# Kernel optimization log

Hardware: AMD Instinct MI355X
Metric: run time of the kernel (lower is better)

The kernel has to match this reference:

```python
import jax, jax.numpy as jnp
import numpy as np

B, T, D = 4, 2048, 2048
NUM_HEADS = 16
NUM_KV_HEADS = 4
HEAD_DIM = D // NUM_HEADS  # 128
KV_GROUPS = NUM_HEADS // NUM_KV_HEADS  # 4
ROPE_THETA = 10000.0


def _rope_tables(seq_len, head_dim, theta):
    inv_freq = 1.0 / theta ** (jnp.arange(0, head_dim, 2, dtype=jnp.float32) / head_dim)
    t = jnp.arange(seq_len, dtype=jnp.float32)
    freqs = jnp.outer(t, inv_freq)  # (T, head_dim//2)
    return jnp.cos(freqs), jnp.sin(freqs)


def _apply_rotary(x, cos, sin):
    # x: (B, H, T, d); cos/sin: (T, d//2)
    d = x.shape[-1]
    x1, x2 = x[..., : d // 2], x[..., d // 2:]
    c = cos[None, None, :, :]
    s = sin[None, None, :, :]
    return jnp.concatenate([x1 * c - x2 * s, x1 * s + x2 * c], axis=-1)


def setup_inputs() -> dict:
    key = jax.random.key(0)
    kx, kq, kk, kv, ko = jax.random.split(key, 5)
    scale = 1.0 / np.sqrt(D)
    return {
        "x": jax.random.normal(kx, (B, T, D), dtype=jnp.float32),
        "Wq": jax.random.normal(kq, (NUM_HEADS * HEAD_DIM, D), dtype=jnp.float32) * scale,
        "Wk": jax.random.normal(kk, (NUM_KV_HEADS * HEAD_DIM, D), dtype=jnp.float32) * scale,
        "Wv": jax.random.normal(kv, (NUM_KV_HEADS * HEAD_DIM, D), dtype=jnp.float32) * scale,
        "Wo": jax.random.normal(ko, (D, D), dtype=jnp.float32) * scale,
    }


def reference(x, Wq, Wk, Wv, Wo):
    Bc, Tc, Dc = x.shape
    # projections (Linear with weight (out,in): y = x @ W.T)
    q = (x @ Wq.T).reshape(Bc, Tc, NUM_HEADS, HEAD_DIM).transpose(0, 2, 1, 3)
    k = (x @ Wk.T).reshape(Bc, Tc, NUM_KV_HEADS, HEAD_DIM).transpose(0, 2, 1, 3)
    v = (x @ Wv.T).reshape(Bc, Tc, NUM_KV_HEADS, HEAD_DIM).transpose(0, 2, 1, 3)

    cos, sin = _rope_tables(Tc, HEAD_DIM, ROPE_THETA)
    q = _apply_rotary(q, cos, sin)
    k = _apply_rotary(k, cos, sin)

    # grouped-query attention: broadcast KV heads instead of repeat_interleave
    # q: (B, kvH, G, T, d); k,v: (B, kvH, T, d)
    qg = q.reshape(Bc, NUM_KV_HEADS, KV_GROUPS, Tc, HEAD_DIM)
    scores = jnp.einsum("bkgtd,bksd->bkgts", qg, k) / jnp.sqrt(jnp.float32(HEAD_DIM))
    causal = jnp.tril(jnp.ones((Tc, Tc), dtype=bool))
    scores = jnp.where(causal[None, None, None], scores, jnp.float32(-jnp.inf))
    attn = jax.nn.softmax(scores, axis=-1)
    out = jnp.einsum("bkgts,bksd->bkgtd", attn, v)  # (B, kvH, G, T, d)
    out = out.reshape(Bc, NUM_HEADS, Tc, HEAD_DIM).transpose(0, 2, 1, 3).reshape(Bc, Tc, Dc)
    return out @ Wo.T
```

## Files before the change

kernel.cpp:

```cpp
#include <hip/hip_runtime.h>
#include <stdint.h>

#define B_ 4
#define T_ 2048
#define D_ 2048
#define NH_ 16
#define NKV_ 4
#define HD_ 128
#define QKVN 3072
#define SCALE_ 0.08838834764831845f

typedef unsigned short u16;
typedef __attribute__((ext_vector_type(8))) short short8;
typedef __attribute__((ext_vector_type(4))) float floatx4;

typedef __attribute__((address_space(1))) void* gas_p;
typedef __attribute__((address_space(3))) void* las_p;

__device__ __forceinline__ u16 f2bf(float f) {
  union { float f; uint32_t u; } a; a.f = f;
  uint32_t r = a.u + 0x7fffu + ((a.u >> 16) & 1u);
  return (u16)(r >> 16);
}
__device__ __forceinline__ float bf2f(u16 u) {
  union { uint32_t u; float f; } a; a.u = ((uint32_t)u) << 16;
  return a.f;
}
__device__ __forceinline__ void gl_lds16(const u16* g, u16* l) {
  __builtin_amdgcn_global_load_lds((gas_p)g, (las_p)l, 16, 0, 0);
}

__global__ void cvt_kernel(const float* __restrict__ in, u16* __restrict__ out, int n) {
  int i = blockIdx.x * 256 + threadIdx.x;
  if (i * 4 >= n) return;
  float4 v = ((const float4*)in)[i];
  union { u16 u[4]; uint2 v2; } o;
  o.u[0] = f2bf(v.x); o.u[1] = f2bf(v.y); o.u[2] = f2bf(v.z); o.u[3] = f2bf(v.w);
  ((uint2*)out)[i] = o.v2;
}

__global__ void rope_tables_kernel(float* __restrict__ tabs) {
  int i = blockIdx.x * 256 + threadIdx.x;
  if (i >= T_ * 64) return;
  int t = i >> 6, d = i & 63;
  float inv = powf(10000.0f, -(float)d / 64.0f);
  float f = (float)t * inv;
  tabs[i] = cosf(f);
  tabs[T_ * 64 + i] = sinf(f);
}

__global__ void rope_q_kernel(const u16* __restrict__ qkv, const float* __restrict__ tabs,
                              u16* __restrict__ q_r) {
  int i = blockIdx.x * 256 + threadIdx.x;
  if (i >= B_ * T_ * NH_ * 64) return;
  int d = i & 63;
  int h = (i >> 6) & 15;
  int t = (i >> 10) & 2047;
  int b = i >> 21;
  size_t row = (size_t)(b * T_ + t) * QKVN + h * HD_;
  float x1 = bf2f(qkv[row + d]);
  float x2 = bf2f(qkv[row + d + 64]);
  float c = tabs[t * 64 + d];
  float s = tabs[T_ * 64 + t * 64 + d];
  size_t ob = ((size_t)(b * NH_ + h) * T_ + t) * HD_;
  q_r[ob + d] = f2bf((x1 * c - x2 * s) * SCALE_);
  q_r[ob + d + 64] = f2bf((x1 * s + x2 * c) * SCALE_);
}

__global__ void rope_k_kernel(const u16* __restrict__ qkv, const float* __restrict__ tabs,
                              u16* __restrict__ k_r) {
  int i = blockIdx.x * 256 + threadIdx.x;
  if (i >= B_ * T_ * NKV_ * 64) return;
  int d = i & 63;
  int kh = (i >> 6) & 3;
  int t = (i >> 8) & 2047;
  int b = i >> 19;
  size_t row = (size_t)(b * T_ + t) * QKVN + D_ + kh * HD_;
  float x1 = bf2f(qkv[row + d]);
  float x2 = bf2f(qkv[row + d + 64]);
  float c = tabs[t * 64 + d];
  float s = tabs[T_ * 64 + t * 64 + d];
  size_t ob = ((size_t)(b * NKV_ + kh) * T_ + t) * HD_;
  k_r[ob + d] = f2bf(x1 * c - x2 * s);
  k_r[ob + d + 64] = f2bf(x1 * s + x2 * c);
}

__global__ void v_trans_kernel(const u16* __restrict__ qkv, u16* __restrict__ v_t) {
  __shared__ u16 tile[64 * 128];
  int bk = blockIdx.y;
  int b = bk >> 2, kh = bk & 3;
  int t0 = blockIdx.x * 64;
#pragma unroll
  for (int rep = 0; rep < 32; rep++) {
    int idx = rep * 256 + threadIdx.x;
    int tt = idx >> 7, d = idx & 127;
    tile[idx] = qkv[(size_t)(b * T_ + t0 + tt) * QKVN + D_ + 512 + kh * HD_ + d];
  }
  __syncthreads();
#pragma unroll
  for (int rep = 0; rep < 32; rep++) {
    int idx = rep * 256 + threadIdx.x;
    int d = idx >> 6, tt = idx & 63;
    v_t[((size_t)bk * HD_ + d) * T_ + t0 + tt] = tile[tt * 128 + d];
  }
}

template <int OUTF32>
__global__ __launch_bounds__(256)
void gemm_bt(const u16* __restrict__ A, const u16* __restrict__ Bm,
             void* __restrict__ Cv, int M, int N, int K) {
  __shared__ u16 As[128 * 64];
  __shared__ u16 Bs[128 * 64];
  const int tid = threadIdx.x;
  const int wave = tid >> 6, lane = tid & 63;
  const int l16 = lane & 15, quad = lane >> 4;
  const int m0 = blockIdx.y * 128, n0 = blockIdx.x * 128;
  const int wm = (wave >> 1) * 64, wn = (wave & 1) * 64;

  floatx4 acc[4][4];
#pragma unroll
  for (int i = 0; i < 4; i++)
#pragma unroll
    for (int j = 0; j < 4; j++)
#pragma unroll
      for (int r = 0; r < 4; r++) acc[i][j][r] = 0.0f;

  const u16* gA[4]; const u16* gB[4]; u16* lA[4]; u16* lB[4];
#pragma unroll
  for (int rep = 0; rep < 4; rep++) {
    int u = rep * 256 + tid;
    int row = u >> 3;
    int ks = (u & 7) ^ (row & 7);
    gA[rep] = A + (size_t)(m0 + row) * K + ks * 8;
    gB[rep] = Bm + (size_t)(n0 + row) * K + ks * 8;
    lA[rep] = &As[u * 8];
    lB[rep] = &Bs[u * 8];
  }

  for (int k0 = 0; k0 < K; k0 += 64) {
#pragma unroll
    for (int rep = 0; rep < 4; rep++) {
      gl_lds16(gA[rep] + k0, lA[rep]);
      gl_lds16(gB[rep] + k0, lB[rep]);
    }
    __syncthreads();
#pragma unroll
    for (int kc = 0; kc < 2; kc++) {
      const int kq = (kc * 4 + quad) ^ (l16 & 7);
      short8 af[4], bfv[4];
#pragma unroll
      for (int i = 0; i < 4; i++)
        af[i] = *(const short8*)(As + ((wm + i * 16 + l16) * 8 + kq) * 8);
#pragma unroll
      for (int j = 0; j < 4; j++)
        bfv[j] = *(const short8*)(Bs + ((wn + j * 16 + l16) * 8 + kq) * 8);
#pragma unroll
      for (int i = 0; i < 4; i++)
#pragma unroll
        for (int j = 0; j < 4; j++)
          acc[i][j] = __builtin_amdgcn_mfma_f32_16x16x32_bf16(af[i], bfv[j], acc[i][j], 0, 0, 0);
    }
    __syncthreads();
  }
#pragma unroll
  for (int i = 0; i < 4; i++)
#pragma unroll
    for (int j = 0; j < 4; j++)
#pragma unroll
      for (int r = 0; r < 4; r++) {
        int m = m0 + wm + i * 16 + quad * 4 + r;
        int n = n0 + wn + j * 16 + l16;
        if (OUTF32)
          ((float*)Cv)[(size_t)m * N + n] = acc[i][j][r];
        else
          ((u16*)Cv)[(size_t)m * N + n] = f2bf(acc[i][j][r]);
      }
}

__global__ __launch_bounds__(256)
void attn_fused(const u16* __restrict__ q_r, const u16* __restrict__ k_r,
                const u16* __restrict__ v_t, u16* __restrict__ outp) {
  __shared__ u16 Ks[64 * 128];
  __shared__ u16 Vs[64 * 128];
  __shared__ u16 Ps[4][32 * 64];
  const int tid = threadIdx.x;
  const int wave = tid >> 6, lane = tid & 63;
  const int l16 = lane & 15, quad = lane >> 4;
  const int bh = blockIdx.y;
  const int b = bh >> 4, h = bh & 15;
  const int kh = h >> 2;

  const u16* qhead = q_r + (size_t)bh * T_ * HD_;
  const u16* khead = k_r + (size_t)(b * NKV_ + kh) * T_ * HD_;
  const u16* vhead = v_t + (size_t)(b * NKV_ + kh) * HD_ * T_;

  int uu[4], kv_j[4], kv_kb[4], v_jo[4], v_k2[4], nn16[4], qq[4];
#pragma unroll
  for (int rep = 0; rep < 4; rep++) {
    int u = rep * 256 + tid;
    uu[rep] = u;
    nn16[rep] = u & 15; qq[rep] = (u >> 4) & 3;
    kv_j[rep] = (u >> 6) & 3; kv_kb[rep] = (u >> 8) & 3;
    v_jo[rep] = (u >> 6) & 7; v_k2[rep] = (u >> 9) & 1;
  }

  const short8 ones = { 0x3F80, 0x3F80, 0x3F80, 0x3F80, 0x3F80, 0x3F80, 0x3F80, 0x3F80 };
  u16* psw = &Ps[wave][0];

  for (int pass = 0; pass < 2; pass++) {
    const int qtile = pass ? (15 - (int)blockIdx.x) : (int)blockIdx.x;
    const int qbase = qtile * 128;
    const int ntiles = 2 * qtile + 2;

    short8 qf[2][4];
#pragma unroll
    for (int i = 0; i < 2; i++) {
      int t = qbase + wave * 32 + i * 16 + l16;
#pragma unroll
      for (int kb = 0; kb < 4; kb++)
        qf[i][kb] = *(const short8*)(qhead + (size_t)t * HD_ + kb * 32 + quad * 8);
    }

    const u16* kg[4]; const u16* vg[4]; u16* kl[4]; u16* vl[4];
#pragma unroll
    for (int rep = 0; rep < 4; rep++) {
      kg[rep] = khead + (size_t)(kv_j[rep] * 16 + nn16[rep]) * HD_ + kv_kb[rep] * 32 + qq[rep] * 8;
      vg[rep] = vhead + (size_t)(v_jo[rep] * 16 + nn16[rep]) * T_ + v_k2[rep] * 32 + qq[rep] * 8;
      kl[rep] = &Ks[uu[rep] * 8];
      vl[rep] = &Vs[uu[rep] * 8];
    }

    floatx4 acc_o[2][8];
    floatx4 acc_l[2];
#pragma unroll
    for (int i = 0; i < 2; i++) {
#pragma unroll
      for (int jo = 0; jo < 8; jo++)
#pragma unroll
        for (int r = 0; r < 4; r++) acc_o[i][jo][r] = 0.0f;
#pragma unroll
      for (int r = 0; r < 4; r++) acc_l[i][r] = 0.0f;
    }

    for (int tile = 0; tile < ntiles; tile++) {
      const int kv0 = tile * 64;
#pragma unroll
      for (int rep = 0; rep < 4; rep++) {
        gl_lds16(kg[rep], kl[rep]);
        gl_lds16(vg[rep], vl[rep]);
        kg[rep] += 64 * HD_;
        vg[rep] += 64;
      }
      __syncthreads();

      floatx4 s_acc[2][4];
#pragma unroll
      for (int i = 0; i < 2; i++)
#pragma unroll
        for (int j = 0; j < 4; j++)
#pragma unroll
          for (int r = 0; r < 4; r++) s_acc[i][j][r] = 0.0f;
#pragma unroll
      for (int kb = 0; kb < 4; kb++) {
        short8 bk[4];
#pragma unroll
        for (int j = 0; j < 4; j++)
          bk[j] = *(const short8*)(Ks + (((kb * 4 + j) * 4 + quad) * 16 + l16) * 8);
#pragma unroll
        for (int i = 0; i < 2; i++)
#pragma unroll
          for (int j = 0; j < 4; j++)
            s_acc[i][j] = __builtin_amdgcn_mfma_f32_16x16x32_bf16(qf[i][kb], bk[j], s_acc[i][j], 0, 0, 0);
      }

      if (tile + 2 >= ntiles) {
#pragma unroll
        for (int i = 0; i < 2; i++)
#pragma unroll
          for (int j = 0; j < 4; j++) {
            const int col = kv0 + j * 16 + l16;
            const int k = j * 16 + l16;
#pragma unroll
            for (int r = 0; r < 4; r++) {
              const int qrow = qbase + wave * 32 + i * 16 + quad * 4 + r;
              float p = (col > qrow) ? 0.0f : __expf(s_acc[i][j][r]);
              int addr = (((i * 2 + (k >> 5)) * 4 + ((k >> 3) & 3)) * 16 + quad * 4 + r) * 8 + (k & 7);
              psw[addr] = f2bf(p);
            }
          }
      } else {
#pragma unroll
        for (int i = 0; i < 2; i++)
#pragma unroll
          for (int j = 0; j < 4; j++) {
            const int k = j * 16 + l16;
#pragma unroll
            for (int r = 0; r < 4; r++) {
              float p = __expf(s_acc[i][j][r]);
              int addr = (((i * 2 + (k >> 5)) * 4 + ((k >> 3) & 3)) * 16 + quad * 4 + r) * 8 + (k & 7);
              psw[addr] = f2bf(p);
            }
          }
      }

#pragma unroll
      for (int k2 = 0; k2 < 2; k2++) {
        short8 ap[2];
#pragma unroll
        for (int i = 0; i < 2; i++)
          ap[i] = *(const short8*)(psw + (((i * 2 + k2) * 4 + quad) * 16 + l16) * 8);
#pragma unroll
        for (int jo = 0; jo < 8; jo++) {
          short8 bv = *(const short8*)(Vs + (((k2 * 8 + jo) * 4 + quad) * 16 + l16) * 8);
          acc_o[0][jo] = __builtin_amdgcn_mfma_f32_16x16x32_bf16(ap[0], bv, acc_o[0][jo], 0, 0, 0);
          acc_o[1][jo] = __builtin_amdgcn_mfma_f32_16x16x32_bf16(ap[1], bv, acc_o[1][jo], 0, 0, 0);
        }
        acc_l[0] = __builtin_amdgcn_mfma_f32_16x16x32_bf16(ap[0], ones, acc_l[0], 0, 0, 0);
        acc_l[1] = __builtin_amdgcn_mfma_f32_16x16x32_bf16(ap[1], ones, acc_l[1], 0, 0, 0);
      }
      __syncthreads();
    }

#pragma unroll
    for (int i = 0; i < 2; i++)
#pragma unroll
      for (int r = 0; r < 4; r++) {
        const float inv = 1.0f / acc_l[i][r];
        const int t = qbase + wave * 32 + i * 16 + quad * 4 + r;
        u16* orow = outp + ((size_t)(b * T_ + t)) * D_ + h * HD_;
#pragma unroll
        for (int jo = 0; jo < 8; jo++)
          orow[jo * 16 + l16] = f2bf(acc_o[i][jo][r] * inv);
      }
    __syncthreads();
  }
}

extern "C" void kernel_launch(void* const* d_in, const int* in_sizes, int n_in,
                              void* d_out, int out_size, void* d_ws, size_t ws_size,
                              hipStream_t stream) {
  const float* x  = (const float*)d_in[0];
  const float* Wq = (const float*)d_in[1];
  const float* Wk = (const float*)d_in[2];
  const float* Wv = (const float*)d_in[3];
  const float* Wo = (const float*)d_in[4];

  char* ws = (char*)d_ws;
  u16* xbf  = (u16*)(ws);
  u16* attn = xbf;
  u16* qkv  = (u16*)(ws + 33554432);
  u16* wcat = (u16*)(ws + 83886080);
  u16* wobf = (u16*)(ws + 96468992);
  u16* qr   = (u16*)(ws + 104857600);
  u16* kr   = (u16*)(ws + 138412032);
  u16* vt   = (u16*)(ws + 146800640);
  float* tabs = (float*)(ws + 155189248);

  cvt_kernel<<<16384, 256, 0, stream>>>(x, xbf, 16777216);
  cvt_kernel<<<4096, 256, 0, stream>>>(Wq, wcat, 4194304);
  cvt_kernel<<<1024, 256, 0, stream>>>(Wk, wcat + 4194304, 1048576);
  cvt_kernel<<<1024, 256, 0, stream>>>(Wv, wcat + 5242880, 1048576);
  cvt_kernel<<<4096, 256, 0, stream>>>(Wo, wobf, 4194304);
  rope_tables_kernel<<<512, 256, 0, stream>>>(tabs);

  gemm_bt<0><<<dim3(24, 64), 256, 0, stream>>>(xbf, wcat, (void*)qkv, 8192, 3072, 2048);

  rope_q_kernel<<<32768, 256, 0, stream>>>(qkv, tabs, qr);
  rope_k_kernel<<<8192, 256, 0, stream>>>(qkv, tabs, kr);
  v_trans_kernel<<<dim3(32, 16), 256, 0, stream>>>(qkv, vt);

  attn_fused<<<dim3(8, 64), 256, 0, stream>>>(qr, kr, vt, attn);

  gemm_bt<1><<<dim3(16, 64), 256, 0, stream>>>(attn, wobf, d_out, 8192, 2048, 2048);
}
```

Measured before the change: 485.5 us.

## Double-buffer K/V tiles in attention to overlap loads with MFMA compute

The attention kernel now keeps two LDS buffers for K and V and issues the global-to-LDS loads for the next KV tile before computing on the current one. It waits only for the older batch of loads using a partial vmcnt wait and plain s_barrier calls instead of __syncthreads. The aim is to hide global memory latency behind the QK and PV MFMA work. In exchange LDS use grows to about 80KB per block, which may lower occupancy, and correctness depends on the hand-written vmcnt counts.

```diff
diff --git a/kernel.cpp b/kernel.cpp
--- a/kernel.cpp
+++ b/kernel.cpp
@@ -180,8 +180,8 @@
 __global__ __launch_bounds__(256)
 void attn_fused(const u16* __restrict__ q_r, const u16* __restrict__ k_r,
                 const u16* __restrict__ v_t, u16* __restrict__ outp) {
-  __shared__ u16 Ks[64 * 128];
-  __shared__ u16 Vs[64 * 128];
+  __shared__ u16 Ks[2][64 * 128];
+  __shared__ u16 Vs[2][64 * 128];
   __shared__ u16 Ps[4][32 * 64];
   const int tid = threadIdx.x;
   const int wave = tid >> 6, lane = tid & 63;
@@ -221,13 +221,11 @@
         qf[i][kb] = *(const short8*)(qhead + (size_t)t * HD_ + kb * 32 + quad * 8);
     }
 
-    const u16* kg[4]; const u16* vg[4]; u16* kl[4]; u16* vl[4];
+    const u16* kg[4]; const u16* vg[4];
 #pragma unroll
     for (int rep = 0; rep < 4; rep++) {
       kg[rep] = khead + (size_t)(kv_j[rep] * 16 + nn16[rep]) * HD_ + kv_kb[rep] * 32 + qq[rep] * 8;
       vg[rep] = vhead + (size_t)(v_jo[rep] * 16 + nn16[rep]) * T_ + v_k2[rep] * 32 + qq[rep] * 8;
-      kl[rep] = &Ks[uu[rep] * 8];
-      vl[rep] = &Vs[uu[rep] * 8];
     }
 
     floatx4 acc_o[2][8];
@@ -242,16 +240,34 @@
       for (int r = 0; r < 4; r++) acc_l[i][r] = 0.0f;
     }
 
+#pragma unroll
+    for (int rep = 0; rep < 4; rep++) {
+      gl_lds16(kg[rep], &Ks[0][uu[rep] * 8]);
+      gl_lds16(vg[rep], &Vs[0][uu[rep] * 8]);
+      kg[rep] += 64 * HD_;
+      vg[rep] += 64;
+    }
+
     for (int tile = 0; tile < ntiles; tile++) {
       const int kv0 = tile * 64;
-#pragma unroll
-      for (int rep = 0; rep < 4; rep++) {
-        gl_lds16(kg[rep], kl[rep]);
-        gl_lds16(vg[rep], vl[rep]);
-        kg[rep] += 64 * HD_;
-        vg[rep] += 64;
-      }
-      __syncthreads();
+      const int cur = tile & 1;
+      if (tile + 1 < ntiles) {
+#pragma unroll
+        for (int rep = 0; rep < 4; rep++) {
+          gl_lds16(kg[rep], &Ks[cur ^ 1][uu[rep] * 8]);
+          gl_lds16(vg[rep], &Vs[cur ^ 1][uu[rep] * 8]);
+          kg[rep] += 64 * HD_;
+          vg[rep] += 64;
+        }
+        asm volatile("s_waitcnt vmcnt(8)" ::: "memory");
+      } else {
+        asm volatile("s_waitcnt vmcnt(0)" ::: "memory");
+      }
+      __builtin_amdgcn_s_barrier();
+      __builtin_amdgcn_sched_barrier(0);
+
+      const u16* ksb = &Ks[cur][0];
+      const u16* vsb = &Vs[cur][0];
 
       floatx4 s_acc[2][4];
 #pragma unroll
@@ -265,7 +281,7 @@
         short8 bk[4];
 #pragma unroll
         for (int j = 0; j < 4; j++)
-          bk[j] = *(const short8*)(Ks + (((kb * 4 + j) * 4 + quad) * 16 + l16) * 8);
+          bk[j] = *(const short8*)(ksb + (((kb * 4 + j) * 4 + quad) * 16 + l16) * 8);
 #pragma unroll
         for (int i = 0; i < 2; i++)
 #pragma unroll
@@ -311,14 +327,15 @@
           ap[i] = *(const short8*)(psw + (((i * 2 + k2) * 4 + quad) * 16 + l16) * 8);
 #pragma unroll
         for (int jo = 0; jo < 8; jo++) {
-          short8 bv = *(const short8*)(Vs + (((k2 * 8 + jo) * 4 + quad) * 16 + l16) * 8);
+          short8 bv = *(const short8*)(vsb + (((k2 * 8 + jo) * 4 + quad) * 16 + l16) * 8);
           acc_o[0][jo] = __builtin_amdgcn_mfma_f32_16x16x32_bf16(ap[0], bv, acc_o[0][jo], 0, 0, 0);
           acc_o[1][jo] = __builtin_amdgcn_mfma_f32_16x16x32_bf16(ap[1], bv, acc_o[1][jo], 0, 0, 0);
         }
         acc_l[0] = __builtin_amdgcn_mfma_f32_16x16x32_bf16(ap[0], ones, acc_l[0], 0, 0, 0);
         acc_l[1] = __builtin_amdgcn_mfma_f32_16x16x32_bf16(ap[1], ones, acc_l[1], 0, 0, 0);
       }
-      __syncthreads();
+      __builtin_amdgcn_sched_barrier(0);
+      __builtin_amdgcn_s_barrier();
     }
 
 #pragma unroll
```

Result: slower. 561.0 us (+15.6%).

## Transpose QK MFMA, pack P stores with swizzled LDS layout, use exp2

Applied to the files above, without the earlier changes.

The QK^T MFMA operands are swapped so each lane holds four consecutive key columns for one query row. These are packed with v_cvt_pk_bf16_f32 and written as 8-byte stores into an XOR-swizzled LDS layout for P, replacing sixteen scalar 2-byte stores. The q scale now folds in log2(e) so exp2f replaces __expf. s_setprio raises wave priority around the MFMA blocks. This cuts LDS store traffic and bank conflicts in the softmax-to-PV handoff, at the cost of a scale baked into q that slightly changes bf16 rounding.

```diff
diff --git a/kernel.cpp b/kernel.cpp
--- a/kernel.cpp
+++ b/kernel.cpp
@@ -8,7 +8,7 @@
 #define NKV_ 4
 #define HD_ 128
 #define QKVN 3072
-#define SCALE_ 0.08838834764831845f
+#define QSCALE_ 0.1275174334161689f
 
 typedef unsigned short u16;
 typedef __attribute__((ext_vector_type(8))) short short8;
@@ -63,8 +63,8 @@
   float c = tabs[t * 64 + d];
   float s = tabs[T_ * 64 + t * 64 + d];
   size_t ob = ((size_t)(b * NH_ + h) * T_ + t) * HD_;
-  q_r[ob + d] = f2bf((x1 * c - x2 * s) * SCALE_);
-  q_r[ob + d + 64] = f2bf((x1 * s + x2 * c) * SCALE_);
+  q_r[ob + d] = f2bf((x1 * c - x2 * s) * QSCALE_);
+  q_r[ob + d + 64] = f2bf((x1 * s + x2 * c) * QSCALE_);
 }
 
 __global__ void rope_k_kernel(const u16* __restrict__ qkv, const float* __restrict__ tabs,
@@ -205,7 +205,8 @@
   }
 
   const short8 ones = { 0x3F80, 0x3F80, 0x3F80, 0x3F80, 0x3F80, 0x3F80, 0x3F80, 0x3F80 };
-  u16* psw = &Ps[wave][0];
+  char* psb = (char*)&Ps[wave][0];
+  const int swz = (l16 & 7) << 4;
 
   for (int pass = 0; pass < 2; pass++) {
     const int qtile = pass ? (15 - (int)blockIdx.x) : (int)blockIdx.x;
@@ -260,6 +261,7 @@
         for (int j = 0; j < 4; j++)
 #pragma unroll
           for (int r = 0; r < 4; r++) s_acc[i][j][r] = 0.0f;
+      __builtin_amdgcn_s_setprio(1);
 #pragma unroll
       for (int kb = 0; kb < 4; kb++) {
         short8 bk[4];
@@ -270,45 +272,57 @@
         for (int i = 0; i < 2; i++)
 #pragma unroll
           for (int j = 0; j < 4; j++)
-            s_acc[i][j] = __builtin_amdgcn_mfma_f32_16x16x32_bf16(qf[i][kb], bk[j], s_acc[i][j], 0, 0, 0);
-      }
+            s_acc[i][j] = __builtin_amdgcn_mfma_f32_16x16x32_bf16(bk[j], qf[i][kb], s_acc[i][j], 0, 0, 0);
+      }
+      __builtin_amdgcn_s_setprio(0);
 
       if (tile + 2 >= ntiles) {
 #pragma unroll
-        for (int i = 0; i < 2; i++)
+        for (int i = 0; i < 2; i++) {
+          const int qg = qbase + wave * 32 + i * 16 + l16;
+          const int prow = i * 16 + l16;
 #pragma unroll
           for (int j = 0; j < 4; j++) {
-            const int col = kv0 + j * 16 + l16;
-            const int k = j * 16 + l16;
-#pragma unroll
-            for (int r = 0; r < 4; r++) {
-              const int qrow = qbase + wave * 32 + i * 16 + quad * 4 + r;
-              float p = (col > qrow) ? 0.0f : __expf(s_acc[i][j][r]);
-              int addr = (((i * 2 + (k >> 5)) * 4 + ((k >> 3) & 3)) * 16 + quad * 4 + r) * 8 + (k & 7);
-              psw[addr] = f2bf(p);
-            }
+            const int kg0 = kv0 + j * 16 + quad * 4;
+            float p0 = (kg0 + 0 > qg) ? 0.0f : exp2f(s_acc[i][j][0]);
+            float p1 = (kg0 + 1 > qg) ? 0.0f : exp2f(s_acc[i][j][1]);
+            float p2 = (kg0 + 2 > qg) ? 0.0f : exp2f(s_acc[i][j][2]);
+            float p3 = (kg0 + 3 > qg) ? 0.0f : exp2f(s_acc[i][j][3]);
+            uint32_t lo, hi;
+            asm("v_cvt_pk_bf16_f32 %0, %1, %2" : "=v"(lo) : "v"(p0), "v"(p1));
+            asm("v_cvt_pk_bf16_f32 %0, %1, %2" : "=v"(hi) : "v"(p2), "v"(p3));
+            uint2 pk; pk.x = lo; pk.y = hi;
+            *(uint2*)(psb + ((prow * 128 + j * 32 + quad * 8) ^ swz)) = pk;
           }
+        }
       } else {
 #pragma unroll
-        for (int i = 0; i < 2; i++)
+        for (int i = 0; i < 2; i++) {
+          const int prow = i * 16 + l16;
 #pragma unroll
           for (int j = 0; j < 4; j++) {
-            const int k = j * 16 + l16;
-#pragma unroll
-            for (int r = 0; r < 4; r++) {
-              float p = __expf(s_acc[i][j][r]);
-              int addr = (((i * 2 + (k >> 5)) * 4 + ((k >> 3) & 3)) * 16 + quad * 4 + r) * 8 + (k & 7);
-              psw[addr] = f2bf(p);
-            }
+            float p0 = exp2f(s_acc[i][j][0]);
+            float p1 = exp2f(s_acc[i][j][1]);
+            float p2 = exp2f(s_acc[i][j][2]);
+            float p3 = exp2f(s_acc[i][j][3]);
+            uint32_t lo, hi;
+            asm("v_cvt_pk_bf16_f32 %0, %1, %2" : "=v"(lo) : "v"(p0), "v"(p1));
+            asm("v_cvt_pk_bf16_f32 %0, %1, %2" : "=v"(hi) : "v"(p2), "v"(p3));
+            uint2 pk; pk.x = lo; pk.y = hi;
+            *(uint2*)(psb + ((prow * 128 + j * 32 + quad * 8) ^ swz)) = pk;
           }
-      }
-
+        }
+      }
+
+      __builtin_amdgcn_s_setprio(1);
 #pragma unroll
       for (int k2 = 0; k2 < 2; k2++) {
         short8 ap[2];
 #pragma unroll
-        for (int i = 0; i < 2; i++)
-          ap[i] = *(const short8*)(psw + (((i * 2 + k2) * 4 + quad) * 16 + l16) * 8);
+        for (int i = 0; i < 2; i++) {
+          const int prow = i * 16 + l16;
+          ap[i] = *(const short8*)(psb + ((prow * 128 + k2 * 64 + quad * 16) ^ swz));
+        }
 #pragma unroll
         for (int jo = 0; jo < 8; jo++) {
           short8 bv = *(const short8*)(Vs + (((k2 * 8 + jo) * 4 + quad) * 16 + l16) * 8);
@@ -318,6 +332,7 @@
         acc_l[0] = __builtin_amdgcn_mfma_f32_16x16x32_bf16(ap[0], ones, acc_l[0], 0, 0, 0);
         acc_l[1] = __builtin_amdgcn_mfma_f32_16x16x32_bf16(ap[1], ones, acc_l[1], 0, 0, 0);
       }
+      __builtin_amdgcn_s_setprio(0);
       __syncthreads();
     }
 
```

Result: slower. 500.8 us (+3.2%).
